# Kernel optimization log

Hardware: AMD Instinct MI355X
Metric: run time of the kernel (lower is better)

The kernel has to match this reference:

```python
import jax, jax.numpy as jnp
import numpy as np

B, D, H, W = 16, 384, 64, 64
Dq, Dv, NH, DFF = 768, 384, 12, 1536
EPS = 1e-5


def setup_inputs() -> dict:
    key = jax.random.key(0)
    ks = jax.random.split(key, 8)

    def w(k, out_c, in_c):
        return (jax.random.normal(k, (out_c, in_c), jnp.float32) / np.float32(np.sqrt(in_c)))

    return {
        "x": jax.random.normal(ks[0], (B, D, H, W), jnp.float32),
        "ln1_w": jnp.ones((D, H, W), jnp.float32),
        "ln1_b": jnp.zeros((D, H, W), jnp.float32),
        "qw": w(ks[1], Dq, D), "qb": jnp.zeros((Dq,), jnp.float32),
        "kw": w(ks[2], Dq, D), "kb": jnp.zeros((Dq,), jnp.float32),
        "vw": w(ks[3], Dv, D), "vb": jnp.zeros((Dv,), jnp.float32),
        "hu_w": w(ks[4], D, Dv), "hu_b": jnp.zeros((D,), jnp.float32),
        "ln2_w": jnp.ones((D, H, W), jnp.float32),
        "ln2_b": jnp.zeros((D, H, W), jnp.float32),
        "ff1_w": w(ks[5], DFF, D), "ff1_b": jnp.zeros((DFF,), jnp.float32),
        "ff2_w": w(ks[6], D, DFF), "ff2_b": jnp.zeros((D,), jnp.float32),
    }


def layernorm(x, w, b):
    # torch.nn.LayerNorm((D, H, W)): normalize over last 3 dims, biased var
    mu = x.mean(axis=(1, 2, 3), keepdims=True)
    var = x.var(axis=(1, 2, 3), keepdims=True)
    return (x - mu) * jax.lax.rsqrt(var + EPS) * w + b


def conv1x1(x, w, b):
    # 1x1 conv == channel-mixing matmul; x: (B, Cin, H, W), w: (Cout, Cin)
    return jnp.einsum('bdhw,od->bohw', x, w) + b[None, :, None, None]


def reference(x, ln1_w, ln1_b, qw, qb, kw, kb, vw, vb, hu_w, hu_b,
              ln2_w, ln2_b, ff1_w, ff1_b, ff2_w, ff2_b):
    a = layernorm(x, ln1_w, ln1_b)
    Q = conv1x1(a, qw, qb)  # (B, Dq, H, W)
    K = conv1x1(a, kw, kb)  # (B, Dq, H, W)
    V = conv1x1(a, vw, vb)  # (B, Dv, H, W)

    Q = jax.nn.softmax(Q, axis=1)  # softmax over channels (subtract-max is built in)
    K = jax.nn.softmax(K.reshape(B, Dq, H * W), axis=-1).reshape(B, Dq, H, W)

    Qh = Q.reshape(B, NH, Dq // NH, H, W)
    Kh = K.reshape(B, NH, Dq // NH, H, W)
    Vh = V.reshape(B, NH, Dv // NH, H, W)

    # kernel_size=1: adaptive_avg_pool2d(KV, 1) * 1 == spatial mean of K (x) V,
    # and the grouped 1x1 conv is a per-(batch,head) (Dv/h x Dq/h) matmul on Q.
    KV = jnp.einsum('bhqyx,bhvyx->bhqv', Kh, Vh) / np.float32(H * W)
    QKV = jnp.einsum('bhqv,bhqyx->bhvyx', KV, Qh).reshape(B, Dv, H, W)

    attn = conv1x1(QKV, hu_w, hu_b)  # head unification, (B, D, H, W)
    x = x + attn
    x = layernorm(x, ln2_w, ln2_b)
    ff = conv1x1(jax.nn.gelu(conv1x1(x, ff1_w, ff1_b), approximate=False), ff2_w, ff2_b)
    return x + ff
```

## Files before the change

kernel.cpp:

```cpp
#include <hip/hip_runtime.h>
#include <hip/hip_bf16.h>

using u16 = unsigned short;
typedef __attribute__((ext_vector_type(4))) float f32x4;
typedef __bf16 bf16x8 __attribute__((ext_vector_type(8)));
typedef short s16x4 __attribute__((ext_vector_type(4)));
typedef short s16x8 __attribute__((ext_vector_type(8)));

#define DEVI __device__ __forceinline__

DEVI float b2f(u16 u) {
    union { unsigned i; float f; } x; x.i = ((unsigned)u) << 16; return x.f;
}
DEVI u16 f2b(float f) {
    union { float f; unsigned i; } x; x.f = f;
    unsigned r = (x.i + 0x7fffu + ((x.i >> 16) & 1u)) >> 16;
    return (u16)r;
}

DEVI float gelu_fast(float v) {
    float t = v * (1.5957691f + 0.0713548162f * v * v);
    return v / (1.f + __expf(-t));
}

static constexpr long long PX = 1572864LL;
static constexpr long long PQ = 3145728LL;
static constexpr long long PH = 6291456LL;

DEVI void gl_lds16(const u16* g, u16* l) {
    __builtin_amdgcn_global_load_lds(
        (const __attribute__((address_space(1))) unsigned int*)g,
        (__attribute__((address_space(3))) unsigned int*)l, 16, 0, 0);
}

__global__ __launch_bounds__(256)
void wconv_kernel(const float* __restrict__ qw, const float* __restrict__ kw,
                  const float* __restrict__ vw, const float* __restrict__ huw,
                  const float* __restrict__ ff1w, const float* __restrict__ ff2w,
                  u16* __restrict__ wcv)
{
    int blk = blockIdx.x;
    const float* src; u16* dst; int lb;
    if      (blk < 288)  { src = qw;   dst = wcv;           lb = blk; }
    else if (blk < 576)  { src = kw;   dst = wcv + 294912;  lb = blk - 288; }
    else if (blk < 720)  { src = vw;   dst = wcv + 589824;  lb = blk - 576; }
    else if (blk < 864)  { src = huw;  dst = wcv + 737280;  lb = blk - 720; }
    else if (blk < 1440) { src = ff1w; dst = wcv + 884736;  lb = blk - 864; }
    else                 { src = ff2w; dst = wcv + 1474560; lb = blk - 1440; }
    int i = (lb * 256 + threadIdx.x) * 4;
    f32x4 v = *(const f32x4*)(src + i);
    s16x4 o;
#pragma unroll
    for (int j = 0; j < 4; ++j) o[j] = (short)f2b(v[j]);
    *(s16x4*)(dst + i) = o;
}

__global__ __launch_bounds__(256)
void bcat_kernel(const float* __restrict__ qb, const float* __restrict__ kb,
                 const float* __restrict__ vb, float* __restrict__ o)
{
    int i = blockIdx.x * 256 + threadIdx.x;
    if (i < 768)       o[i] = qb[i];
    else if (i < 1536) o[i] = kb[i - 768];
    else if (i < 1920) o[i] = vb[i - 1536];
}

__global__ __launch_bounds__(256, 4)
void gemm_qkv_kernel(const u16* __restrict__ A, long long strideA,
                     const u16* __restrict__ Bw,
                     const float* __restrict__ bias,
                     u16* __restrict__ Q, u16* __restrict__ Kd, u16* __restrict__ V,
                     float* __restrict__ rsump, int K)
{
    const int tid = threadIdx.x;
    const int lane = tid & 63;
    const int wv = tid >> 6;
    const int wr = wv >> 1, wc = wv & 1;
    const int l15 = lane & 15, l4 = lane >> 4;
    const int bm = blockIdx.x, bn = blockIdx.y, bz = blockIdx.z;

    A += (long long)bz * strideA;
    u16* dstBase; int Nout; int colBase;
    if (bn < 6)       { dstBase = Q  + (long long)bz * PQ; Nout = 768; colBase = bn * 128; }
    else if (bn < 12) { dstBase = Kd + (long long)bz * PQ; Nout = 768; colBase = (bn - 6) * 128; }
    else              { dstBase = V  + (long long)bz * PX; Nout = 384; colBase = (bn - 12) * 128; }
    const bool isQ = (bn < 6);

    __shared__ u16 lds[2][128 * 64];

    f32x4 acc[4][4] = {};

    auto stage = [&](int kt) {
#pragma unroll
        for (int i = 0; i < 4; ++i) {
            int cid = tid + i * 256;
            int row = cid >> 3, c8 = cid & 7;
            int c8s = c8 ^ (row & 7);
            gl_lds16(A + (long long)(bm * 128 + row) * K + kt + c8s * 8,
                     &lds[0][cid * 8]);
        }
#pragma unroll
        for (int i = 0; i < 4; ++i) {
            int cid = tid + i * 256;
            int row = cid >> 3, c8 = cid & 7;
            int c8s = c8 ^ (row & 7);
            gl_lds16(Bw + (long long)(bn * 128 + row) * K + kt + c8s * 8,
                     &lds[1][cid * 8]);
        }
    };

    auto compute = [&]() {
#pragma unroll
        for (int kk = 0; kk < 2; ++kk) {
            bf16x8 af[4], bfr[4];
#pragma unroll
            for (int mi = 0; mi < 4; ++mi) {
                int row = wr * 64 + mi * 16 + l15;
                int idx8 = (kk * 4 + l4) ^ (row & 7);
                af[mi] = *(const bf16x8*)&lds[0][row * 64 + idx8 * 8];
            }
#pragma unroll
            for (int ni = 0; ni < 4; ++ni) {
                int row = wc * 64 + ni * 16 + l15;
                int idx8 = (kk * 4 + l4) ^ (row & 7);
                bfr[ni] = *(const bf16x8*)&lds[1][row * 64 + idx8 * 8];
            }
#pragma unroll
            for (int mi = 0; mi < 4; ++mi)
#pragma unroll
                for (int ni = 0; ni < 4; ++ni)
                    acc[mi][ni] = __builtin_amdgcn_mfma_f32_16x16x32_bf16(af[mi], bfr[ni], acc[mi][ni], 0, 0, 0);
        }
    };

    stage(0);
    asm volatile("s_waitcnt vmcnt(0)" ::: "memory");
    __syncthreads();
    for (int kt = 64; kt < K; kt += 64) {
        compute();
        __syncthreads();
        stage(kt);
        asm volatile("s_waitcnt vmcnt(0)" ::: "memory");
        __syncthreads();
    }
    compute();

    u16* st = &lds[0][0];
#pragma unroll
    for (int p = 0; p < 2; ++p) {
        __syncthreads();
        if (wr == p) {
#pragma unroll
            for (int ni = 0; ni < 4; ++ni) {
                int colL = wc * 64 + ni * 16 + l15;
                float bv = bias[bn * 128 + colL];
#pragma unroll
                for (int mi = 0; mi < 4; ++mi) {
#pragma unroll
                    for (int r = 0; r < 4; ++r) {
                        float v = acc[mi][ni][r] + bv;
                        if (isQ) v = __expf(v);
                        st[(mi * 16 + l4 * 4 + r) * 136 + colL] = f2b(v);
                    }
                }
            }
        }
        __syncthreads();
        int lr = tid >> 2, q = tid & 3;
        const u16* src = st + lr * 136 + q * 32;
        u16* dst = dstBase + (long long)(bm * 128 + p * 64 + lr) * Nout + colBase + q * 32;
        float s = 0.f;
#pragma unroll
        for (int j = 0; j < 4; ++j) {
            s16x8 v8 = *(const s16x8*)(src + j * 8);
            *(s16x8*)(dst + j * 8) = v8;
            if (isQ) {
#pragma unroll
                for (int e = 0; e < 8; ++e) s += b2f((u16)v8[e]);
            }
        }
        if (isQ) {
            s += __shfl_xor(s, 1);
            s += __shfl_xor(s, 2);
            if (q == 0)
                rsump[((long long)(bz * 6 + bn)) * 4096 + bm * 128 + p * 64 + lr] = s;
        }
    }
}

__global__ __launch_bounds__(256, 4)
void gemm_attn_kernel(const u16* __restrict__ A, long long strideA,
                      const u16* __restrict__ Bw, long long strideB,
                      const float* __restrict__ bias,
                      const float* __restrict__ x,
                      const float* __restrict__ rsump,
                      u16* __restrict__ sT,
                      float* __restrict__ part2, int K)
{
    const int tid = threadIdx.x;
    const int lane = tid & 63;
    const int wv = tid >> 6;
    const int wr = wv >> 1, wc = wv & 1;
    const int l15 = lane & 15, l4 = lane >> 4;
    const int bm = blockIdx.x, bn = blockIdx.y, bz = blockIdx.z;

    A  += (long long)bz * strideA;
    Bw += (long long)bz * strideB;
    x  += (long long)bz * PX;
    sT += (long long)bz * PX;

    __shared__ u16 lds[2][128 * 64];
    __shared__ float sscale[128];

    if (tid < 128) {
        float s = 0.f;
#pragma unroll
        for (int j = 0; j < 6; ++j)
            s += rsump[((long long)(bz * 6 + j)) * 4096 + bm * 128 + tid];
        sscale[tid] = 1.f / s;
    }

    f32x4 acc[4][4] = {};

    auto stage = [&](int kt) {
#pragma unroll
        for (int i = 0; i < 4; ++i) {
            int cid = tid + i * 256;
            int row = cid >> 3, c8 = cid & 7;
            int c8s = c8 ^ (row & 7);
            gl_lds16(A + (long long)(bm * 128 + row) * K + kt + c8s * 8,
                     &lds[0][cid * 8]);
        }
#pragma unroll
        for (int i = 0; i < 4; ++i) {
            int cid = tid + i * 256;
            int row = cid >> 3, c8 = cid & 7;
            int c8s = c8 ^ (row & 7);
            gl_lds16(Bw + (long long)(bn * 128 + row) * K + kt + c8s * 8,
                     &lds[1][cid * 8]);
        }
    };

    auto compute = [&]() {
#pragma unroll
        for (int kk = 0; kk < 2; ++kk) {
            bf16x8 af[4], bfr[4];
#pragma unroll
            for (int mi = 0; mi < 4; ++mi) {
                int row = wr * 64 + mi * 16 + l15;
                int idx8 = (kk * 4 + l4) ^ (row & 7);
                af[mi] = *(const bf16x8*)&lds[0][row * 64 + idx8 * 8];
            }
#pragma unroll
            for (int ni = 0; ni < 4; ++ni) {
                int row = wc * 64 + ni * 16 + l15;
                int idx8 = (kk * 4 + l4) ^ (row & 7);
                bfr[ni] = *(const bf16x8*)&lds[1][row * 64 + idx8 * 8];
            }
#pragma unroll
            for (int mi = 0; mi < 4; ++mi)
#pragma unroll
                for (int ni = 0; ni < 4; ++ni)
                    acc[mi][ni] = __builtin_amdgcn_mfma_f32_16x16x32_bf16(af[mi], bfr[ni], acc[mi][ni], 0, 0, 0);
        }
    };

    stage(0);
    asm volatile("s_waitcnt vmcnt(0)" ::: "memory");
    __syncthreads();
    for (int kt = 64; kt < K; kt += 64) {
        compute();
        __syncthreads();
        stage(kt);
        asm volatile("s_waitcnt vmcnt(0)" ::: "memory");
        __syncthreads();
    }
    compute();

    u16* st = &lds[0][0];
    float ps = 0.f, pq = 0.f;
#pragma unroll
    for (int p = 0; p < 2; ++p) {
        __syncthreads();
        if (wr == p) {
#pragma unroll
            for (int ni = 0; ni < 4; ++ni) {
                int colL = wc * 64 + ni * 16 + l15;
                int colG = bn * 128 + colL;
                float bv = bias[colG];
#pragma unroll
                for (int mi = 0; mi < 4; ++mi) {
                    const float* xp = x + (long long)colG * 4096 + bm * 128 + p * 64 + mi * 16 + l4 * 4;
                    f32x4 xv = *(const f32x4*)xp;
#pragma unroll
                    for (int r = 0; r < 4; ++r) {
                        float ss = sscale[p * 64 + mi * 16 + l4 * 4 + r];
                        st[(mi * 16 + l4 * 4 + r) * 136 + colL] = f2b(acc[mi][ni][r] * ss + bv + xv[r]);
                    }
                }
            }
        }
        __syncthreads();
        int lr = tid >> 2, q = tid & 3;
        const u16* src = st + lr * 136 + q * 32;
        u16* dst = sT + (long long)(bm * 128 + p * 64 + lr) * 384 + bn * 128 + q * 32;
#pragma unroll
        for (int j = 0; j < 4; ++j) {
            s16x8 v = *(const s16x8*)(src + j * 8);
            *(s16x8*)(dst + j * 8) = v;
#pragma unroll
            for (int e = 0; e < 8; ++e) { float f = b2f((u16)v[e]); ps += f; pq += f * f; }
        }
    }

    for (int off = 32; off; off >>= 1) { ps += __shfl_down(ps, off); pq += __shfl_down(pq, off); }
    __shared__ float rs[4], rq[4];
    if (lane == 0) { rs[wv] = ps; rq[wv] = pq; }
    __syncthreads();
    if (tid == 0) {
        int bid = bz * 96 + bm * 3 + bn;
        part2[bid * 2 + 0] = rs[0] + rs[1] + rs[2] + rs[3];
        part2[bid * 2 + 1] = rq[0] + rq[1] + rq[2] + rq[3];
    }
}

__global__ __launch_bounds__(256, 4)
void gemm_bt_kernel(const u16* __restrict__ A, long long strideA,
                    const u16* __restrict__ Bw, long long strideB,
                    const float* __restrict__ bias,
                    u16* __restrict__ C, long long strideC,
                    float* __restrict__ Cf,
                    const u16* __restrict__ addT, long long strideAdd,
                    int K, int N, int doGelu)
{
    const int tid = threadIdx.x;
    const int lane = tid & 63;
    const int wv = tid >> 6;
    const int wr = wv >> 1, wc = wv & 1;
    const int l15 = lane & 15, l4 = lane >> 4;
    const int bm = blockIdx.x, bn = blockIdx.y, bz = blockIdx.z;

    A  += (long long)bz * strideA;
    Bw += (long long)bz * strideB;
    if (C)    C    += (long long)bz * strideC;
    if (Cf)   Cf   += (long long)bz * strideC;
    if (addT) addT += (long long)bz * strideAdd;

    __shared__ u16 lds[2][128 * 64];

    f32x4 acc[4][4] = {};

    auto stage = [&](int kt) {
#pragma unroll
        for (int i = 0; i < 4; ++i) {
            int cid = tid + i * 256;
            int row = cid >> 3, c8 = cid & 7;
            int c8s = c8 ^ (row & 7);
            gl_lds16(A + (long long)(bm * 128 + row) * K + kt + c8s * 8,
                     &lds[0][cid * 8]);
        }
#pragma unroll
        for (int i = 0; i < 4; ++i) {
            int cid = tid + i * 256;
            int row = cid >> 3, c8 = cid & 7;
            int c8s = c8 ^ (row & 7);
            gl_lds16(Bw + (long long)(bn * 128 + row) * K + kt + c8s * 8,
                     &lds[1][cid * 8]);
        }
    };

    auto compute = [&]() {
#pragma unroll
        for (int kk = 0; kk < 2; ++kk) {
            bf16x8 af[4], bfr[4];
#pragma unroll
            for (int mi = 0; mi < 4; ++mi) {
                int row = wr * 64 + mi * 16 + l15;
                int idx8 = (kk * 4 + l4) ^ (row & 7);
                af[mi] = *(const bf16x8*)&lds[0][row * 64 + idx8 * 8];
            }
#pragma unroll
            for (int ni = 0; ni < 4; ++ni) {
                int row = wc * 64 + ni * 16 + l15;
                int idx8 = (kk * 4 + l4) ^ (row & 7);
                bfr[ni] = *(const bf16x8*)&lds[1][row * 64 + idx8 * 8];
            }
#pragma unroll
            for (int mi = 0; mi < 4; ++mi)
#pragma unroll
                for (int ni = 0; ni < 4; ++ni)
                    acc[mi][ni] = __builtin_amdgcn_mfma_f32_16x16x32_bf16(af[mi], bfr[ni], acc[mi][ni], 0, 0, 0);
        }
    };

    stage(0);
    asm volatile("s_waitcnt vmcnt(0)" ::: "memory");
    __syncthreads();
    for (int kt = 64; kt < K; kt += 64) {
        compute();
        __syncthreads();
        stage(kt);
        asm volatile("s_waitcnt vmcnt(0)" ::: "memory");
        __syncthreads();
    }
    compute();

    if (!Cf) {
        u16* st = &lds[0][0];
#pragma unroll
        for (int p = 0; p < 2; ++p) {
            __syncthreads();
            if (wr == p) {
#pragma unroll
                for (int ni = 0; ni < 4; ++ni) {
                    int colL = wc * 64 + ni * 16 + l15;
                    float bv = bias ? bias[bn * 128 + colL] : 0.f;
#pragma unroll
                    for (int mi = 0; mi < 4; ++mi) {
#pragma unroll
                        for (int r = 0; r < 4; ++r) {
                            float v = acc[mi][ni][r] + bv;
                            if (doGelu) v = gelu_fast(v);
                            st[(mi * 16 + l4 * 4 + r) * 136 + colL] = f2b(v);
                        }
                    }
                }
            }
            __syncthreads();
            int lr = tid >> 2, q = tid & 3;
            const u16* src = st + lr * 136 + q * 32;
            u16* dst = C + (long long)(bm * 128 + p * 64 + lr) * N + bn * 128 + q * 32;
#pragma unroll
            for (int j = 0; j < 4; ++j)
                *(s16x8*)(dst + j * 8) = *(const s16x8*)(src + j * 8);
        }
    } else {
        float* stf = (float*)&lds[0][0];
#pragma unroll
        for (int p = 0; p < 4; ++p) {
            __syncthreads();
            if (wc == (p >> 1)) {
#pragma unroll
                for (int nj = 0; nj < 2; ++nj) {
                    int ni = (p & 1) * 2 + nj;
                    int colL = wc * 64 + ni * 16 + l15;
                    int lc = nj * 16 + l15;
                    float bv = bias ? bias[bn * 128 + colL] : 0.f;
#pragma unroll
                    for (int mi = 0; mi < 4; ++mi) {
                        int row0 = wr * 64 + mi * 16 + l4 * 4;
#pragma unroll
                        for (int r = 0; r < 4; ++r) {
                            float v = acc[mi][ni][r] + bv
                                    + b2f(addT[(long long)(bm * 128 + row0 + r) * N + bn * 128 + colL]);
                            stf[lc * 132 + row0 + r] = v;
                        }
                    }
                }
            }
            __syncthreads();
            int lc = tid >> 3, q = tid & 7;
            float* dst = Cf + (long long)(bn * 128 + p * 32 + lc) * 4096 + bm * 128 + q * 16;
            const float* src = stf + lc * 132 + q * 16;
#pragma unroll
            for (int j = 0; j < 4; ++j)
                *(f32x4*)(dst + j * 4) = *(const f32x4*)(src + j * 4);
        }
    }
}

__global__ __launch_bounds__(256)
void stats_part_kernel(const float* __restrict__ x, float* __restrict__ part)
{
    int b = blockIdx.x, cb = blockIdx.y, t = threadIdx.x;
    const float* p = x + (long long)b * PX + (long long)cb * 49152;
    float s = 0.f, q = 0.f;
    for (int i = 0; i < 48; ++i) {
        f32x4 v = *(const f32x4*)(p + (i * 256 + t) * 4);
#pragma unroll
        for (int j = 0; j < 4; ++j) { s += v[j]; q += v[j] * v[j]; }
    }
    for (int off = 32; off; off >>= 1) { s += __shfl_down(s, off); q += __shfl_down(q, off); }
    __shared__ float rs[4], rq[4];
    if ((t & 63) == 0) { rs[t >> 6] = s; rq[t >> 6] = q; }
    __syncthreads();
    if (t == 0) {
        part[(b * 32 + cb) * 2 + 0] = rs[0] + rs[1] + rs[2] + rs[3];
        part[(b * 32 + cb) * 2 + 1] = rq[0] + rq[1] + rq[2] + rq[3];
    }
}

__global__ void stats_fin_kernel(const float* __restrict__ part, float* __restrict__ mu, float* __restrict__ rsg)
{
    int b = blockIdx.x, l = threadIdx.x;
    float s = l < 32 ? part[(b * 32 + l) * 2 + 0] : 0.f;
    float q = l < 32 ? part[(b * 32 + l) * 2 + 1] : 0.f;
    for (int off = 32; off; off >>= 1) { s += __shfl_down(s, off); q += __shfl_down(q, off); }
    if (l == 0) {
        float m = s / 1572864.f;
        float v = q / 1572864.f - m * m; v = fmaxf(v, 0.f);
        mu[b] = m; rsg[b] = rsqrtf(v + 1e-5f);
    }
}

__global__ __launch_bounds__(256)
void ln_apply_T_kernel(const float* __restrict__ src, const float* __restrict__ w, const float* __restrict__ bb,
                       const float* __restrict__ mu, const float* __restrict__ rsg, u16* __restrict__ dstT)
{
    int nt = blockIdx.x, dt = blockIdx.y, b = blockIdx.z;
    int t = threadIdx.x, tx = t & 63, ty = t >> 6;
    __shared__ float tile[64][65];
    float m = mu[b], r = rsg[b];
    const long long base = (long long)b * PX;
#pragma unroll 4
    for (int i = 0; i < 16; ++i) {
        int dy = ty + i * 4;
        int d = dt * 64 + dy, n = nt * 64 + tx;
        long long widx = (long long)d * 4096 + n;
        tile[dy][tx] = (src[base + widx] - m) * r * w[widx] + bb[widx];
    }
    __syncthreads();
#pragma unroll 4
    for (int i = 0; i < 16; ++i) {
        int ny = ty + i * 4;
        int n = nt * 64 + ny, d = dt * 64 + tx;
        dstT[base + (long long)n * 384 + d] = f2b(tile[tx][ny]);
    }
}

__global__ __launch_bounds__(256)
void kv_part_kernel(const u16* __restrict__ KT, const u16* __restrict__ VT,
                    u16* __restrict__ KVp, float* __restrict__ sp)
{
    const int ch = blockIdx.x, h = blockIdx.y, b = blockIdx.z;
    const int t = threadIdx.x;
    const int lane = t & 63, w = t >> 6;

    __shared__ u16 kraw[128 * 64];
    __shared__ u16 eKT[64 * 128];
    __shared__ u16 Vt[32 * 128];
    __shared__ float reds[4][64];

    const u16* Kp = KT + (long long)b * PQ + (long long)(ch * 128) * 768 + h * 64;
    const u16* Vp = VT + (long long)b * PX + (long long)(ch * 128) * 384 + h * 32;

#pragma unroll
    for (int pass = 0; pass < 4; ++pass) {
        int cid = t + pass * 256;
        int row = cid >> 3, c8 = cid & 7;
        gl_lds16(Kp + (long long)row * 768 + c8 * 8, kraw + cid * 8);
    }

    {
        int v0 = (t & 7) * 4;
#pragma unroll
        for (int pass = 0; pass < 4; ++pass) {
            int n = (t >> 3) + pass * 32;
            s16x4 v4 = *(const s16x4*)(Vp + (long long)n * 384 + v0);
#pragma unroll
            for (int j = 0; j < 4; ++j) {
                int row = v0 + j;
                Vt[row * 128 + (n ^ ((row & 7) << 3))] = (u16)v4[j];
            }
        }
    }

    asm volatile("s_waitcnt vmcnt(0)" ::: "memory");
    __syncthreads();

    const int c = lane;
    {
        float s = 0.f;
        const int swz = (c & 7) << 3;
#pragma unroll
        for (int r8 = 0; r8 < 4; ++r8) {
            int rbase = w * 32 + r8 * 8;
            s16x8 buf;
#pragma unroll
            for (int j = 0; j < 8; ++j) {
                float e = __expf(b2f(kraw[(rbase + j) * 64 + c]));
                s += e;
                buf[j] = (short)f2b(e);
            }
            *(s16x8*)&eKT[c * 128 + (rbase ^ swz)] = buf;
        }
        reds[w][c] = s;
    }
    __syncthreads();

    if (t < 64)
        sp[((long long)(b * 12 + h) * 32 + ch) * 64 + t] =
            reds[0][t] + reds[1][t] + reds[2][t] + reds[3][t];

    const int l15 = lane & 15, l4 = lane >> 4;
    const int qrow = w * 16 + l15;
    const int sa = (qrow & 7) << 3;
    const int v0row = l15, v1row = 16 + l15;
    const int s0 = (v0row & 7) << 3, s1 = (v1row & 7) << 3;
    f32x4 acc0 = {}, acc1 = {};
#pragma unroll
    for (int ns = 0; ns < 4; ++ns) {
        int na = ns * 32 + l4 * 8;
        bf16x8 a  = *(const bf16x8*)&eKT[qrow * 128 + (na ^ sa)];
        bf16x8 b0 = *(const bf16x8*)&Vt[v0row * 128 + (na ^ s0)];
        bf16x8 b1 = *(const bf16x8*)&Vt[v1row * 128 + (na ^ s1)];
        acc0 = __builtin_amdgcn_mfma_f32_16x16x32_bf16(a, b0, acc0, 0, 0, 0);
        acc1 = __builtin_amdgcn_mfma_f32_16x16x32_bf16(a, b1, acc1, 0, 0, 0);
    }
    u16* Kb = KVp + ((long long)(b * 12 + h) * 32 + ch) * 2048;
#pragma unroll
    for (int r = 0; r < 4; ++r) {
        int q = w * 16 + l4 * 4 + r;
        Kb[q * 32 + l15]      = f2b(acc0[r]);
        Kb[q * 32 + 16 + l15] = f2b(acc1[r]);
    }
}

__global__ __launch_bounds__(256)
void kv_fin_kernel(const u16* __restrict__ KVp, const float* __restrict__ sp,
                   const u16* __restrict__ huwB, u16* __restrict__ Wcomb)
{
    const int h = blockIdx.x, b = blockIdx.y;
    const int t = threadIdx.x;
    const int lane = t & 63, w = t >> 6;
    const int l15 = lane & 15, l4 = lane >> 4;

    __shared__ float fac[64];
    __shared__ u16 kvq[64 * 40];
    __shared__ u16 hw[384 * 40];

    for (int i = t; i < 384 * 4; i += 256) {
        int row = i >> 2, seg = i & 3;
        *(s16x8*)&hw[row * 40 + seg * 8] =
            *(const s16x8*)(huwB + row * 384 + h * 32 + seg * 8);
    }

    const long long pb = (long long)(b * 12 + h) * 32;
    if (t < 64) {
        float s = 0.f;
#pragma unroll
        for (int ch = 0; ch < 32; ++ch) s += sp[(pb + ch) * 64 + t];
        fac[t] = 1.f / (s * 4096.f);
    }
    __syncthreads();

    {
        const int v0 = (t & 3) * 8, q = t >> 2;
        float acc[8] = {};
#pragma unroll
        for (int ch = 0; ch < 32; ++ch) {
            s16x8 kv8 = *(const s16x8*)&KVp[(pb + ch) * 2048 + q * 32 + v0];
#pragma unroll
            for (int j = 0; j < 8; ++j) acc[j] += b2f((u16)kv8[j]);
        }
        float fq = fac[q];
        s16x8 o;
#pragma unroll
        for (int j = 0; j < 8; ++j) o[j] = (short)f2b(acc[j] * fq);
        *(s16x8*)&kvq[q * 40 + v0] = o;
    }
    __syncthreads();

    bf16x8 af[6], bfr[4];
#pragma unroll
    for (int mi = 0; mi < 6; ++mi)
        af[mi] = *(const bf16x8*)&hw[(w * 96 + mi * 16 + l15) * 40 + l4 * 8];
#pragma unroll
    for (int ni = 0; ni < 4; ++ni)
        bfr[ni] = *(const bf16x8*)&kvq[(ni * 16 + l15) * 40 + l4 * 8];
    f32x4 acc[6][4] = {};
#pragma unroll
    for (int mi = 0; mi < 6; ++mi)
#pragma unroll
        for (int ni = 0; ni < 4; ++ni)
            acc[mi][ni] = __builtin_amdgcn_mfma_f32_16x16x32_bf16(af[mi], bfr[ni], acc[mi][ni], 0, 0, 0);

    u16* Wb = Wcomb + (long long)b * 294912;
#pragma unroll
    for (int mi = 0; mi < 6; ++mi) {
#pragma unroll
        for (int ni = 0; ni < 4; ++ni) {
            int col = h * 64 + ni * 16 + l15;
#pragma unroll
            for (int r = 0; r < 4; ++r) {
                int o = w * 96 + mi * 16 + l4 * 4 + r;
                Wb[o * 768 + col] = f2b(acc[mi][ni][r]);
            }
        }
    }
}

__global__ __launch_bounds__(256)
void wtrans_kernel(const float* __restrict__ w, const float* __restrict__ bb,
                   u16* __restrict__ wT, u16* __restrict__ bT)
{
    int nt = blockIdx.x, dt = blockIdx.y;
    const float* src = blockIdx.z ? bb : w;
    u16* dst = blockIdx.z ? bT : wT;
    int t = threadIdx.x, tx = t & 63, ty = t >> 6;
    __shared__ float tile[64][65];
#pragma unroll 4
    for (int i = 0; i < 16; ++i) {
        int dy = ty + i * 4;
        tile[dy][tx] = src[(long long)(dt * 64 + dy) * 4096 + nt * 64 + tx];
    }
    __syncthreads();
#pragma unroll 4
    for (int i = 0; i < 16; ++i) {
        int ny = ty + i * 4;
        dst[(long long)(nt * 64 + ny) * 384 + dt * 64 + tx] = f2b(tile[tx][ny]);
    }
}

__global__ __launch_bounds__(256)
void stats_fin2_kernel(const float* __restrict__ part2, float* __restrict__ mu, float* __restrict__ rsg)
{
    int b = blockIdx.x, t = threadIdx.x;
    float s = 0.f, q = 0.f;
    if (t < 96) { s = part2[(b * 96 + t) * 2]; q = part2[(b * 96 + t) * 2 + 1]; }
    for (int off = 32; off; off >>= 1) { s += __shfl_down(s, off); q += __shfl_down(q, off); }
    __shared__ float rs[4], rq[4];
    if ((t & 63) == 0) { rs[t >> 6] = s; rq[t >> 6] = q; }
    __syncthreads();
    if (t == 0) {
        float S = rs[0] + rs[1] + rs[2] + rs[3], Q = rq[0] + rq[1] + rq[2] + rq[3];
        float m = S / 1572864.f;
        float v = Q / 1572864.f - m * m; v = fmaxf(v, 0.f);
        mu[b] = m; rsg[b] = rsqrtf(v + 1e-5f);
    }
}

__global__ __launch_bounds__(256)
void ln2_apply_kernel(const u16* __restrict__ sT, const u16* __restrict__ wT, const u16* __restrict__ bT,
                      const float* __restrict__ mu, const float* __restrict__ rsg, u16* __restrict__ x2T)
{
    int blk = blockIdx.x, b = blockIdx.y, t = threadIdx.x;
    float m = mu[b], r = rsg[b];
    long long wi = (long long)blk * 2048 + t * 8;
    long long gi = (long long)b * PX + wi;
    s16x8 sv = *(const s16x8*)(sT + gi);
    s16x8 wv = *(const s16x8*)(wT + wi);
    s16x8 bv = *(const s16x8*)(bT + wi);
    s16x8 o;
#pragma unroll
    for (int j = 0; j < 8; ++j)
        o[j] = (short)f2b((b2f((u16)sv[j]) - m) * r * b2f((u16)wv[j]) + b2f((u16)bv[j]));
    *(s16x8*)(x2T + gi) = o;
}

extern "C" void kernel_launch(void* const* d_in, const int* in_sizes, int n_in,
                              void* d_out, int out_size, void* d_ws, size_t ws_size,
                              hipStream_t stream)
{
    const float* x    = (const float*)d_in[0];
    const float* ln1w = (const float*)d_in[1];
    const float* ln1b = (const float*)d_in[2];
    const float* qw   = (const float*)d_in[3];
    const float* qb   = (const float*)d_in[4];
    const float* kw   = (const float*)d_in[5];
    const float* kb   = (const float*)d_in[6];
    const float* vw   = (const float*)d_in[7];
    const float* vb   = (const float*)d_in[8];
    const float* huw  = (const float*)d_in[9];
    const float* hub  = (const float*)d_in[10];
    const float* ln2w = (const float*)d_in[11];
    const float* ln2b = (const float*)d_in[12];
    const float* ff1w = (const float*)d_in[13];
    const float* ff1b = (const float*)d_in[14];
    const float* ff2w = (const float*)d_in[15];
    const float* ff2b = (const float*)d_in[16];
    float* out = (float*)d_out;

    char* ws = (char*)d_ws;
    u16*   aT    = (u16*)(ws + 0);
    u16*   QT    = (u16*)(ws + 50331648LL);
    u16*   KT    = (u16*)(ws + 150994944LL);
    u16*   VT    = (u16*)(ws + 251658240LL);
    float* rsump = (float*)(ws + 301989888LL);
    u16*   wcv   = (u16*)(ws + 311427072LL);
    float* fbuf  = (float*)(ws + 315555840LL);

    u16*   KVp    = (u16*)(ws + 0);
    float* sp     = (float*)(ws + 25165824LL);
    u16*   WcombB = (u16*)(ws + 27525120LL);

    u16* sT = KT;
    u16* wT = (u16*)(ws + 150994944LL + 50331648LL);
    u16* bT = (u16*)(ws + 150994944LL + 53477376LL);
    u16* g8 = KT;

    u16* x2T = QT;

    u16* qwB   = wcv;
    u16* ff1wB = wcv + 884736;
    u16* ff2wB = wcv + 1474560;
    u16* huwB  = wcv + 737280;

    float* part1 = fbuf;
    float* mu1   = fbuf + 1024;
    float* rs1   = fbuf + 1040;
    float* part2 = fbuf + 1056;
    float* mu2   = part2 + 3072;
    float* rs2   = mu2 + 16;
    float* qkvb  = rs2 + 16;

    wconv_kernel<<<2016, 256, 0, stream>>>(qw, kw, vw, huw, ff1w, ff2w, wcv);
    bcat_kernel<<<8, 256, 0, stream>>>(qb, kb, vb, qkvb);

    stats_part_kernel<<<dim3(16, 32), 256, 0, stream>>>(x, part1);
    stats_fin_kernel<<<16, 64, 0, stream>>>(part1, mu1, rs1);
    ln_apply_T_kernel<<<dim3(64, 6, 16), 256, 0, stream>>>(x, ln1w, ln1b, mu1, rs1, aT);

    gemm_qkv_kernel<<<dim3(32, 15, 16), 256, 0, stream>>>(aT, PX, qwB, qkvb, QT, KT, VT, rsump, 384);

    kv_part_kernel<<<dim3(32, 12, 16), 256, 0, stream>>>(KT, VT, KVp, sp);

    kv_fin_kernel<<<dim3(12, 16), 256, 0, stream>>>(KVp, sp, huwB, WcombB);

    wtrans_kernel<<<dim3(64, 6, 2), 256, 0, stream>>>(ln2w, ln2b, wT, bT);

    gemm_attn_kernel<<<dim3(32, 3, 16), 256, 0, stream>>>(QT, PQ, WcombB, 294912, hub, x, rsump, sT, part2, 768);

    stats_fin2_kernel<<<16, 256, 0, stream>>>(part2, mu2, rs2);
    ln2_apply_kernel<<<dim3(768, 16), 256, 0, stream>>>(sT, wT, bT, mu2, rs2, x2T);

    for (int c = 0; c < 2; ++c) {
        gemm_bt_kernel<<<dim3(32, 12, 8), 256, 0, stream>>>(
            x2T + (long long)c * 8 * PX, PX, ff1wB, 0, ff1b,
            g8, PH, nullptr, nullptr, 0, 384, 1536, 1);
        gemm_bt_kernel<<<dim3(32, 3, 8), 256, 0, stream>>>(
            g8, PH, ff2wB, 0, ff2b,
            nullptr, PX, out + (long long)c * 8 * PX,
            x2T + (long long)c * 8 * PX, PX, 1536, 384, 0);
    }
}
```

Measured before the change: 693.5 us.

## Merge prep kernels into one launch and run FFN GEMMs over full batch

Folds the weight conversion, bias concatenation and LN2 weight/bias transpose into a single prep kernel, removing two launches. The FFN is no longer split into two half-batch chunks. It now issues one FF1 and one FF2 GEMM over all 16 batches, with the full intermediate in a larger workspace region. This halves the FFN launches and doubles the grid per GEMM for better occupancy. The cost is a relocated workspace layout (wT/bT moved) with a 192MB intermediate, which must not overlap live buffers.

```diff
diff --git a/kernel.cpp b/kernel.cpp
--- a/kernel.cpp
+++ b/kernel.cpp
@@ -34,35 +34,56 @@
 }
 
 __global__ __launch_bounds__(256)
-void wconv_kernel(const float* __restrict__ qw, const float* __restrict__ kw,
-                  const float* __restrict__ vw, const float* __restrict__ huw,
-                  const float* __restrict__ ff1w, const float* __restrict__ ff2w,
-                  u16* __restrict__ wcv)
-{
-    int blk = blockIdx.x;
-    const float* src; u16* dst; int lb;
-    if      (blk < 288)  { src = qw;   dst = wcv;           lb = blk; }
-    else if (blk < 576)  { src = kw;   dst = wcv + 294912;  lb = blk - 288; }
-    else if (blk < 720)  { src = vw;   dst = wcv + 589824;  lb = blk - 576; }
-    else if (blk < 864)  { src = huw;  dst = wcv + 737280;  lb = blk - 720; }
-    else if (blk < 1440) { src = ff1w; dst = wcv + 884736;  lb = blk - 864; }
-    else                 { src = ff2w; dst = wcv + 1474560; lb = blk - 1440; }
-    int i = (lb * 256 + threadIdx.x) * 4;
-    f32x4 v = *(const f32x4*)(src + i);
-    s16x4 o;
-#pragma unroll
-    for (int j = 0; j < 4; ++j) o[j] = (short)f2b(v[j]);
-    *(s16x4*)(dst + i) = o;
-}
-
-__global__ __launch_bounds__(256)
-void bcat_kernel(const float* __restrict__ qb, const float* __restrict__ kb,
-                 const float* __restrict__ vb, float* __restrict__ o)
-{
-    int i = blockIdx.x * 256 + threadIdx.x;
-    if (i < 768)       o[i] = qb[i];
-    else if (i < 1536) o[i] = kb[i - 768];
-    else if (i < 1920) o[i] = vb[i - 1536];
+void prep_kernel(const float* __restrict__ qw, const float* __restrict__ kw,
+                 const float* __restrict__ vw, const float* __restrict__ huw,
+                 const float* __restrict__ ff1w, const float* __restrict__ ff2w,
+                 u16* __restrict__ wcv,
+                 const float* __restrict__ qb, const float* __restrict__ kb,
+                 const float* __restrict__ vb, float* __restrict__ qkvb,
+                 const float* __restrict__ ln2w, const float* __restrict__ ln2b,
+                 u16* __restrict__ wT, u16* __restrict__ bT)
+{
+    __shared__ float tile[64][65];
+    int blk = blockIdx.x, t = threadIdx.x;
+    if (blk < 2016) {
+        const float* src; u16* dst; int lb;
+        if      (blk < 288)  { src = qw;   dst = wcv;           lb = blk; }
+        else if (blk < 576)  { src = kw;   dst = wcv + 294912;  lb = blk - 288; }
+        else if (blk < 720)  { src = vw;   dst = wcv + 589824;  lb = blk - 576; }
+        else if (blk < 864)  { src = huw;  dst = wcv + 737280;  lb = blk - 720; }
+        else if (blk < 1440) { src = ff1w; dst = wcv + 884736;  lb = blk - 864; }
+        else                 { src = ff2w; dst = wcv + 1474560; lb = blk - 1440; }
+        int i = (lb * 256 + t) * 4;
+        f32x4 v = *(const f32x4*)(src + i);
+        s16x4 o;
+#pragma unroll
+        for (int j = 0; j < 4; ++j) o[j] = (short)f2b(v[j]);
+        *(s16x4*)(dst + i) = o;
+        return;
+    }
+    if (blk < 2024) {
+        int i = (blk - 2016) * 256 + t;
+        if (i < 768)       qkvb[i] = qb[i];
+        else if (i < 1536) qkvb[i] = kb[i - 768];
+        else if (i < 1920) qkvb[i] = vb[i - 1536];
+        return;
+    }
+    int idx = blk - 2024;
+    int z = idx / 384, rem = idx % 384, dt = rem / 64, nt = rem % 64;
+    const float* src = z ? ln2b : ln2w;
+    u16* dst = z ? bT : wT;
+    int tx = t & 63, ty = t >> 6;
+#pragma unroll 4
+    for (int i = 0; i < 16; ++i) {
+        int dy = ty + i * 4;
+        tile[dy][tx] = src[(long long)(dt * 64 + dy) * 4096 + nt * 64 + tx];
+    }
+    __syncthreads();
+#pragma unroll 4
+    for (int i = 0; i < 16; ++i) {
+        int ny = ty + i * 4;
+        dst[(long long)(nt * 64 + ny) * 384 + dt * 64 + tx] = f2b(tile[tx][ny]);
+    }
 }
 
 __global__ __launch_bounds__(256, 4)
@@ -687,28 +708,6 @@
                 Wb[o * 768 + col] = f2b(acc[mi][ni][r]);
             }
         }
-    }
-}
-
-__global__ __launch_bounds__(256)
-void wtrans_kernel(const float* __restrict__ w, const float* __restrict__ bb,
-                   u16* __restrict__ wT, u16* __restrict__ bT)
-{
-    int nt = blockIdx.x, dt = blockIdx.y;
-    const float* src = blockIdx.z ? bb : w;
-    u16* dst = blockIdx.z ? bT : wT;
-    int t = threadIdx.x, tx = t & 63, ty = t >> 6;
-    __shared__ float tile[64][65];
-#pragma unroll 4
-    for (int i = 0; i < 16; ++i) {
-        int dy = ty + i * 4;
-        tile[dy][tx] = src[(long long)(dt * 64 + dy) * 4096 + nt * 64 + tx];
-    }
-    __syncthreads();
-#pragma unroll 4
-    for (int i = 0; i < 16; ++i) {
-        int ny = ty + i * 4;
-        dst[(long long)(nt * 64 + ny) * 384 + dt * 64 + tx] = f2b(tile[tx][ny]);
     }
 }
 
@@ -785,11 +784,12 @@
     u16*   WcombB = (u16*)(ws + 27525120LL);
 
     u16* sT = KT;
-    u16* wT = (u16*)(ws + 150994944LL + 50331648LL);
-    u16* bT = (u16*)(ws + 150994944LL + 53477376LL);
-    u16* g8 = KT;
+
+    u16* wT = (u16*)(ws + 303562752LL);
+    u16* bT = (u16*)(ws + 306708480LL);
 
     u16* x2T = QT;
+    u16* g16 = (u16*)(ws + 100663296LL);
 
     u16* qwB   = wcv;
     u16* ff1wB = wcv + 884736;
@@ -804,8 +804,8 @@
     float* rs2   = mu2 + 16;
     float* qkvb  = rs2 + 16;
 
-    wconv_kernel<<<2016, 256, 0, stream>>>(qw, kw, vw, huw, ff1w, ff2w, wcv);
-    bcat_kernel<<<8, 256, 0, stream>>>(qb, kb, vb, qkvb);
+    prep_kernel<<<2792, 256, 0, stream>>>(qw, kw, vw, huw, ff1w, ff2w, wcv,
+                                          qb, kb, vb, qkvb, ln2w, ln2b, wT, bT);
 
     stats_part_kernel<<<dim3(16, 32), 256, 0, stream>>>(x, part1);
     stats_fin_kernel<<<16, 64, 0, stream>>>(part1, mu1, rs1);
@@ -814,23 +814,15 @@
     gemm_qkv_kernel<<<dim3(32, 15, 16), 256, 0, stream>>>(aT, PX, qwB, qkvb, QT, KT, VT, rsump, 384);
 
     kv_part_kernel<<<dim3(32, 12, 16), 256, 0, stream>>>(KT, VT, KVp, sp);
-
     kv_fin_kernel<<<dim3(12, 16), 256, 0, stream>>>(KVp, sp, huwB, WcombB);
-
-    wtrans_kernel<<<dim3(64, 6, 2), 256, 0, stream>>>(ln2w, ln2b, wT, bT);
 
     gemm_attn_kernel<<<dim3(32, 3, 16), 256, 0, stream>>>(QT, PQ, WcombB, 294912, hub, x, rsump, sT, part2, 768);
 
     stats_fin2_kernel<<<16, 256, 0, stream>>>(part2, mu2, rs2);
     ln2_apply_kernel<<<dim3(768, 16), 256, 0, stream>>>(sT, wT, bT, mu2, rs2, x2T);
 
-    for (int c = 0; c < 2; ++c) {
-        gemm_bt_kernel<<<dim3(32, 12, 8), 256, 0, stream>>>(
-            x2T + (long long)c * 8 * PX, PX, ff1wB, 0, ff1b,
-            g8, PH, nullptr, nullptr, 0, 384, 1536, 1);
-        gemm_bt_kernel<<<dim3(32, 3, 8), 256, 0, stream>>>(
-            g8, PH, ff2wB, 0, ff2b,
-            nullptr, PX, out + (long long)c * 8 * PX,
-            x2T + (long long)c * 8 * PX, PX, 1536, 384, 0);
-    }
-}
+    gemm_bt_kernel<<<dim3(32, 12, 16), 256, 0, stream>>>(
+        x2T, PX, ff1wB, 0, ff1b, g16, PH, nullptr, nullptr, 0, 384, 1536, 1);
+    gemm_bt_kernel<<<dim3(32, 3, 16), 256, 0, stream>>>(
+        g16, PH, ff2wB, 0, ff2b, nullptr, PX, out, x2T, PX, 1536, 384, 0);
+}
```

New measurement: 696.9 us (median of 2 runs). About the same (+0.5%).
